# Kernel optimization log

Measured on AMD Instinct MI355X. Metric: run time of the kernel, lower is better.

Reference implementation:

```python
import jax, jax.numpy as jnp
import numpy as np

DIM = 256
NUM_HEADS = 8
KERNEL_SIZES = [7, 7]
DILATIONS = [1, 2]
NUM_SPLITS = 2
HEAD_DIM = DIM // NUM_HEADS
SCALE = HEAD_DIM ** -0.5


def _window_start(L, K, D):
    """NATTEN get_window_start, vectorized over indices 0..L-1 (static numpy)."""
    idx = np.arange(L)
    NH = K // 2
    if D <= 1:
        return np.maximum(idx - NH, 0) + (idx + NH >= L) * (L - idx - NH - 1)
    ni = idx - NH * D
    imodd = idx % D
    a = (L // D) * D
    b = L - a
    edge = np.where(imodd < b, L - b + imodd - 2 * NH * D, a + imodd - K * D)
    return np.where(ni < 0, imodd, np.where(idx + NH * D >= L, edge, ni))


def _pb_start(L, K, D):
    """NATTEN get_pb_start (relative position bias offset), static numpy."""
    idx = np.arange(L)
    NH = K // 2
    if D <= 1:
        return NH + (idx < NH) * (NH - idx) + (idx + NH >= L) * (L - idx - 1 - NH)
    return np.where(idx - NH * D < 0, K - 1 - idx // D,
                    np.where(idx + NH * D >= L, (L - idx - 1) // D, NH))


def _natten2d(q, k, v, rpb, K, D):
    # q,k,v: [B,h,H,W,d]; rpb: [h, 2K-1, 2K-1]
    B, h, H, W, d = q.shape
    ki = _window_start(H, K, D)[:, None] + D * np.arange(K)   # [H,K]
    kj = _window_start(W, K, D)[:, None] + D * np.arange(K)   # [W,K]
    bi = _pb_start(H, K, D)[:, None] + np.arange(K)           # [H,K]
    bj = _pb_start(W, K, D)[:, None] + np.arange(K)           # [W,K]
    kg = jnp.take(jnp.take(k, ki, axis=2), kj, axis=4)        # [B,h,H,K,W,K,d]
    vg = jnp.take(jnp.take(v, ki, axis=2), kj, axis=4)        # [B,h,H,K,W,K,d]
    attn = jnp.einsum('bhijd,bhiujvd->bhijuv', q, kg)         # [B,h,H,W,K,K]
    bias = jnp.take(jnp.take(rpb, bi, axis=1), bj, axis=3)    # [h,H,K,W,K]
    attn = attn + bias.transpose(0, 1, 3, 2, 4)[None]
    attn = jax.nn.softmax(attn.reshape(B, h, H, W, K * K), axis=-1)
    attn = attn.reshape(B, h, H, W, K, K)
    return jnp.einsum('bhijuv,bhiujvd->bhijd', attn, vg)      # [B,h,H,W,d]


def setup_inputs() -> dict:
    key = jax.random.key(0)
    ks = jax.random.split(key, 6)
    B, C, H, W = 2, DIM, 56, 56
    x = jax.random.normal(ks[0], (B, C, H, W), dtype=jnp.float32)
    w_qkv1 = jax.random.normal(ks[1], (3 * C, C), dtype=jnp.float32) * (C ** -0.5)
    w_qkv2 = jax.random.normal(ks[2], (3 * C, 1, 3, 3), dtype=jnp.float32) * (1.0 / 3.0)
    rpb0 = jax.random.truncated_normal(ks[3], -2.0, 2.0,
                                       (NUM_HEADS // NUM_SPLITS, 13, 13), dtype=jnp.float32) * 0.02
    rpb1 = jax.random.truncated_normal(ks[4], -2.0, 2.0,
                                       (NUM_HEADS // NUM_SPLITS, 13, 13), dtype=jnp.float32) * 0.02
    w_proj = jax.random.normal(ks[5], (C, C), dtype=jnp.float32) * (C ** -0.5)
    return {"x": x, "w_qkv1": w_qkv1, "w_qkv2": w_qkv2,
            "rpb0": rpb0, "rpb1": rpb1, "w_proj": w_proj}


def reference(x, w_qkv1, w_qkv2, rpb0, rpb1, w_proj):
    B, C, H, W = x.shape
    # qkv: 1x1 conv (no bias) then depthwise 3x3 conv (no bias)
    y = jnp.einsum('oc,bchw->bohw', w_qkv1, x)
    y = jax.lax.conv_general_dilated(
        y, w_qkv2, window_strides=(1, 1), padding='SAME',
        dimension_numbers=('NCHW', 'OIHW', 'NCHW'), feature_group_count=3 * C)
    # Faithful to torch: raw reshape of [B,3C,H,W] -> [B,H,W,3,nh,hd]
    qkv = y.reshape(B, H, W, 3, NUM_HEADS, HEAD_DIM).transpose(3, 0, 4, 1, 2, 5)
    q, k, v = qkv[0] * SCALE, qkv[1], qkv[2]   # [B,nh,H,W,hd]
    hs = NUM_HEADS // NUM_SPLITS
    rpbs = [rpb0, rpb1]
    outs = []
    for s in range(NUM_SPLITS):
        sl = slice(s * hs, (s + 1) * hs)
        outs.append(_natten2d(q[:, sl], k[:, sl], v[:, sl],
                              rpbs[s], KERNEL_SIZES[s], DILATIONS[s]))
    o = jnp.concatenate(outs, axis=1)                 # [B,nh,H,W,hd]
    o = o.transpose(0, 1, 4, 2, 3).reshape(B, C, H, W)
    return jnp.einsum('oc,bchw->bohw', w_proj, o)
```

## Files before the change

kernel.cpp:

```cpp
#include <hip/hip_runtime.h>
#include <hip/hip_bf16.h>

#define HGT 56
#define WID 56
#define SPA 3136
#define CCH 256
#define C3  768
#define NH  8
#define HD  32
#define YB  2408448
#define ISTR 43008
#define JSTR 768
#define SCALE_Q 0.17677669529663687f

typedef __attribute__((ext_vector_type(8))) short short8;
typedef __attribute__((ext_vector_type(4))) float f32x4;

static __device__ __forceinline__ unsigned short f2bf_bits(float f) {
    __hip_bfloat16 h = __float2bfloat16(f);
    union { __hip_bfloat16 h; unsigned short u; } cv; cv.h = h; return cv.u;
}
static __device__ __forceinline__ float bf_lo(unsigned u) {
    union { unsigned x; float f; } c; c.x = u << 16; return c.f;
}
static __device__ __forceinline__ float bf_hi(unsigned u) {
    union { unsigned x; float f; } c; c.x = u & 0xffff0000u; return c.f;
}
static __device__ __forceinline__ float bfu(unsigned short u) {
    union { unsigned x; float f; } c; c.x = (unsigned)u << 16; return c.f;
}
static __device__ __forceinline__ unsigned pk2bf(float a, float b) {
    return ((unsigned)f2bf_bits(b) << 16) | (unsigned)f2bf_bits(a);
}

__global__ __launch_bounds__(256) void k_cvt(const float* __restrict__ x,
                                             const float* __restrict__ w1,
                                             const float* __restrict__ wp,
                                             __hip_bfloat16* __restrict__ xT,
                                             __hip_bfloat16* __restrict__ w1b,
                                             __hip_bfloat16* __restrict__ wpb) {
    __shared__ __align__(16) __hip_bfloat16 Sl[64][80];
    const int t = threadIdx.x;
    const int z = blockIdx.z;
    if (z == 2) {
        const int gid = (blockIdx.y * 49 + blockIdx.x) * 256 + t;
        for (int i = gid * 4; i < 262144; i += 200704) {
            const float* src;
            __hip_bfloat16* dst;
            if (i < 196608) { src = w1 + i; dst = w1b + i; }
            else            { src = wp + (i - 196608); dst = wpb + (i - 196608); }
            float4 v = *(const float4*)src;
            ushort4 u;
            u.x = f2bf_bits(v.x); u.y = f2bf_bits(v.y);
            u.z = f2bf_bits(v.z); u.w = f2bf_bits(v.w);
            *(ushort4*)dst = u;
        }
        return;
    }
    const int b = z, c0 = blockIdx.y * 64, s0 = blockIdx.x * 64;
    const float* xb = x + (size_t)b * (CCH * SPA);
    const int sq = (t & 15) * 4, cq = (t >> 4) * 4;
    float4 r[4];
#pragma unroll
    for (int rr = 0; rr < 4; ++rr)
        r[rr] = *(const float4*)&xb[(size_t)(c0 + cq + rr) * SPA + s0 + sq];
#pragma unroll
    for (int j = 0; j < 4; ++j) {
        ushort4 u;
        u.x = f2bf_bits(((const float*)&r[0])[j]);
        u.y = f2bf_bits(((const float*)&r[1])[j]);
        u.z = f2bf_bits(((const float*)&r[2])[j]);
        u.w = f2bf_bits(((const float*)&r[3])[j]);
        *(ushort4*)&Sl[sq + j][cq] = u;
    }
    __syncthreads();
    const int srow = t >> 2, cslot = t & 3;
    __hip_bfloat16* dst = &xT[(size_t)b * SPA * CCH + (size_t)(s0 + srow) * CCH + c0];
    short8 v0 = *(const short8*)&Sl[srow][cslot * 8];
    short8 v1 = *(const short8*)&Sl[srow][(cslot + 4) * 8];
    *(short8*)&dst[cslot * 8] = v0;
    *(short8*)&dst[(cslot + 4) * 8] = v1;
}

template<bool OBF>
__global__ __launch_bounds__(256) void k_gemm(const __hip_bfloat16* __restrict__ A,
                                              const __hip_bfloat16* __restrict__ B,
                                              void* __restrict__ Cv, int M) {
    __shared__ __align__(16) short sA[4096];
    __shared__ __align__(16) short sB[4096];
    const int t = threadIdx.x;
    const int lane = t & 63, w = t >> 6;
    const int s0 = blockIdx.x * 64, o0 = blockIdx.y * 64, b = blockIdx.z;
    const __hip_bfloat16* Bb = B + (size_t)b * SPA * CCH;

    const int srow = t >> 3;
    const int scol = (t & 7) ^ (srow & 7);
    const char* gA = (const char*)(A  + (size_t)(o0 + srow) * CCH) + scol * 16;
    const char* gB = (const char*)(Bb + (size_t)(s0 + srow) * CCH) + scol * 16;
    char* lA = (char*)sA + w * 1024;
    char* lB = (char*)sB + w * 1024;

    const int wm = w >> 1, wn = w & 1;
    const int lr = lane & 15, kh = lane >> 4;
    const int ar0 = wm * 32 + lr, ar1 = ar0 + 16;
    const int br0 = wn * 32 + lr, br1 = br0 + 16;

    f32x4 acc[2][2] = {};
    for (int kt = 0; kt < 4; ++kt) {
        __builtin_amdgcn_global_load_lds(
            (const __attribute__((address_space(1))) void*)(gA + kt * 128),
            (__attribute__((address_space(3))) void*)lA, 16, 0, 0);
        __builtin_amdgcn_global_load_lds(
            (const __attribute__((address_space(1))) void*)(gA + 16384 + kt * 128),
            (__attribute__((address_space(3))) void*)(lA + 4096), 16, 0, 0);
        __builtin_amdgcn_global_load_lds(
            (const __attribute__((address_space(1))) void*)(gB + kt * 128),
            (__attribute__((address_space(3))) void*)lB, 16, 0, 0);
        __builtin_amdgcn_global_load_lds(
            (const __attribute__((address_space(1))) void*)(gB + 16384 + kt * 128),
            (__attribute__((address_space(3))) void*)(lB + 4096), 16, 0, 0);
        __syncthreads();
#pragma unroll
        for (int kk = 0; kk < 2; ++kk) {
            const int kg = (kk << 2) | kh;
            short8 a0 = *(const short8*)&sA[(ar0 * 128 + ((kg ^ (ar0 & 7)) << 4)) >> 1];
            short8 a1 = *(const short8*)&sA[(ar1 * 128 + ((kg ^ (ar1 & 7)) << 4)) >> 1];
            short8 b0 = *(const short8*)&sB[(br0 * 128 + ((kg ^ (br0 & 7)) << 4)) >> 1];
            short8 b1 = *(const short8*)&sB[(br1 * 128 + ((kg ^ (br1 & 7)) << 4)) >> 1];
            acc[0][0] = __builtin_amdgcn_mfma_f32_16x16x32_bf16(a0, b0, acc[0][0], 0, 0, 0);
            acc[0][1] = __builtin_amdgcn_mfma_f32_16x16x32_bf16(a0, b1, acc[0][1], 0, 0, 0);
            acc[1][0] = __builtin_amdgcn_mfma_f32_16x16x32_bf16(a1, b0, acc[1][0], 0, 0, 0);
            acc[1][1] = __builtin_amdgcn_mfma_f32_16x16x32_bf16(a1, b1, acc[1][1], 0, 0, 0);
        }
        __syncthreads();
    }
#pragma unroll
    for (int mi = 0; mi < 2; ++mi)
#pragma unroll
        for (int ni = 0; ni < 2; ++ni) {
            const int r0 = o0 + wm * 32 + mi * 16 + kh * 4;
            const int cc = s0 + wn * 32 + ni * 16 + lr;
            if constexpr (OBF) {
                __hip_bfloat16* Cb = (__hip_bfloat16*)Cv + (size_t)b * M * SPA;
#pragma unroll
                for (int q = 0; q < 4; ++q)
                    Cb[(size_t)(r0 + q) * SPA + cc] = __float2bfloat16(acc[mi][ni][q]);
            } else {
                float* Cb = (float*)Cv + (size_t)b * M * SPA;
#pragma unroll
                for (int q = 0; q < 4; ++q)
                    Cb[(size_t)(r0 + q) * SPA + cc] = acc[mi][ni][q];
            }
        }
}

__global__ __launch_bounds__(256) void k_dw(const __hip_bfloat16* __restrict__ y1,
                                            const float* __restrict__ w2,
                                            __hip_bfloat16* __restrict__ y2) {
    int idx = blockIdx.x * 256 + threadIdx.x;
    int tw = idx % 14;
    int rest = idx / 14;
    int h = rest % HGT;
    int bc = rest / HGT;
    int w0 = tw * 4;
    const __hip_bfloat16* in = y1 + (size_t)bc * SPA;
    const float* wt = w2 + (bc % C3) * 9;
    float a0 = 0.f, a1 = 0.f, a2 = 0.f, a3 = 0.f;
#pragma unroll
    for (int dh = -1; dh <= 1; ++dh) {
        int hh = h + dh;
        if (hh < 0 || hh >= HGT) continue;
        const __hip_bfloat16* rp = in + hh * WID + w0;
        ushort4 c4 = *(const ushort4*)rp;
        float c0 = bfu(c4.x), c1 = bfu(c4.y), c2 = bfu(c4.z), c3 = bfu(c4.w);
        float l = (w0 > 0)  ? bfu(*(const unsigned short*)(rp - 1)) : 0.f;
        float r = (w0 < 52) ? bfu(*(const unsigned short*)(rp + 4)) : 0.f;
        float wl = wt[(dh + 1) * 3 + 0];
        float wc = wt[(dh + 1) * 3 + 1];
        float wr = wt[(dh + 1) * 3 + 2];
        a0 += wl * l  + wc * c0 + wr * c1;
        a1 += wl * c0 + wc * c1 + wr * c2;
        a2 += wl * c1 + wc * c2 + wr * c3;
        a3 += wl * c2 + wc * c3 + wr * r;
    }
    ushort4 o;
    o.x = f2bf_bits(a0); o.y = f2bf_bits(a1);
    o.z = f2bf_bits(a2); o.w = f2bf_bits(a3);
    *(ushort4*)(y2 + (size_t)bc * SPA + h * WID + w0) = o;
}

template<int D>
__device__ __forceinline__ void attn7_body(short* __restrict__ sK,
                                           short* __restrict__ sVT,
                                           short* __restrict__ sQ,
                                           short* __restrict__ sP,
                                           float* __restrict__ sEB,
                                           const __hip_bfloat16* __restrict__ y2,
                                           const float* __restrict__ rpb,
                                           __hip_bfloat16* __restrict__ opre,
                                           int b, int head, int i, int hsub) {
    const int tid = threadIdx.x;
    const int lane = tid & 63, w = tid >> 6;
    const int lr = lane & 15, kh = lane >> 4;

    int wsi, pbi;
    if (D == 1) {
        wsi = (i < 3) ? 0 : ((i > 52) ? 49 : i - 3);
        pbi = (i < 3) ? 6 - i : ((i > 52) ? 55 - i : 3);
    } else {
        wsi = (i < 6) ? (i & 1) : ((i >= 50) ? 42 + (i & 1) : i - 6);
        pbi = (i < 6) ? 6 - (i >> 1) : ((i >= 50) ? (55 - i) >> 1 : 3);
    }

    const __hip_bfloat16* base  = y2 + (size_t)b * YB + head * HD;
    const __hip_bfloat16* kbase = base + CCH     + wsi * ISTR;
    const __hip_bfloat16* vbase = base + 2 * CCH + wsi * ISTR;
    const __hip_bfloat16* qbase = base + i * ISTR;

    for (int f = tid; f < 1792; f += 256) {
        int u = f >> 8, rem = f & 255, kj = rem >> 2, slot = rem & 3;
        int kjc = (kj > 55) ? 55 : kj;
        const __hip_bfloat16* src = kbase + u * (D * ISTR) + kjc * JSTR + ((slot ^ (kj & 3)) << 3);
        char* dst = (char*)sK + (size_t)(f - lane) * 16;
        __builtin_amdgcn_global_load_lds(
            (const __attribute__((address_space(1))) void*)src,
            (__attribute__((address_space(3))) void*)dst, 16, 0, 0);
    }
    {
        int jq = tid >> 2, slot = tid & 3;
        int jqc = (jq > 55) ? 55 : jq;
        const __hip_bfloat16* src = qbase + jqc * JSTR + ((slot ^ (jq & 3)) << 3);
        char* dst = (char*)sQ + (size_t)(tid - lane) * 16;
        __builtin_amdgcn_global_load_lds(
            (const __attribute__((address_space(1))) void*)src,
            (__attribute__((address_space(3))) void*)dst, 16, 0, 0);
    }
    for (int f = tid; f < 1568; f += 256) {
        int u = f / 224, rem = f - u * 224;
        int dq = rem / 28, kjp = rem - dq * 28;
        const __hip_bfloat16* g0 = vbase + u * (D * ISTR) + (2 * kjp) * JSTR + dq * 4;
        ushort4 va = *(const ushort4*)g0;
        ushort4 vb = *(const ushort4*)(g0 + JSTR);
#pragma unroll
        for (int e = 0; e < 4; ++e) {
            int d = dq * 4 + e;
            unsigned pk = ((unsigned)((&vb.x)[e]) << 16) | (unsigned)((&va.x)[e]);
            int row = u * 32 + d;
            int byt = row * 128 + ((((kjp >> 2) ^ (d & 7)) << 4)) + (kjp & 3) * 4;
            *(unsigned*)((char*)sVT + byt) = pk;
        }
    }
    if (tid < 224) {
        int u = tid >> 5, d = tid & 31;
        int row = u * 32 + d;
        int byt = row * 128 + ((7 ^ (d & 7)) << 4);
        *(short8*)((char*)sVT + byt) = (short8){0, 0, 0, 0, 0, 0, 0, 0};
    }
    if (tid < 91) {
        int u = tid / 13, r = tid - u * 13;
        sEB[tid] = __expf(rpb[hsub * 169 + (pbi + u) * 13 + r]);
    }
    __syncthreads();

    const int j = w * 16 + lr;
    int wsj;
    if (D == 1) wsj = (j < 3) ? 0 : ((j > 52) ? 49 : j - 3);
    else        wsj = (j < 6) ? (j & 1) : ((j >= 50) ? 42 + (j & 1) : j - 6);

    short8 qf = *(const short8*)((char*)sQ + j * 64 + ((kh ^ (j & 3)) << 4));

    float ssum = 0.f;
    f32x4 oacc0 = {0.f, 0.f, 0.f, 0.f};
    f32x4 oacc1 = {0.f, 0.f, 0.f, 0.f};
    short* sPw = sP + w * 2048;

#pragma unroll
    for (int u = 0; u < 7; ++u) {
        char* sPb = (char*)(sPw + (u & 1) * 1024);
        f32x4 s[4];
#pragma unroll
        for (int Mt = 0; Mt < 4; ++Mt) {
            int kjrow = u * 64 + Mt * 16 + lr;
            short8 kf = *(const short8*)((char*)sK + kjrow * 64 + ((kh ^ (lr & 3)) << 4));
            s[Mt] = __builtin_amdgcn_mfma_f32_16x16x32_bf16(kf, qf,
                        (f32x4){0.f, 0.f, 0.f, 0.f}, 0, 0, 0);
        }
#pragma unroll
        for (int Mt = 0; Mt < 4; ++Mt) {
            const int kjb = Mt * 16 + (kh << 2);
            float ev[4];
#pragma unroll
            for (int q = 0; q < 4; ++q) {
                int kj = kjb + q;
                int rel = kj - j;
                int din = kj - wsj;
                bool valid = (din >= 0) && (din <= 6 * D);
                if (D == 2) valid = valid && ((rel & 1) == 0);
                int r = (D == 1) ? (rel + 6) : ((rel >> 1) + 6);
                r = r < 0 ? 0 : (r > 12 ? 12 : r);
                float ex = __expf(s[Mt][q] * SCALE_Q) * sEB[u * 13 + r];
                ev[q] = valid ? ex : 0.f;
                ssum += ev[q];
            }
            uint2 pk2;
            pk2.x = pk2bf(ev[0], ev[1]);
            pk2.y = pk2bf(ev[2], ev[3]);
            int g = Mt * 2 + (kh >> 1);
            int byt = lr * 128 + (((g ^ (lr & 7)) << 4)) + (kh & 1) * 8;
            *(uint2*)(sPb + byt) = pk2;
        }
        __syncthreads();
#pragma unroll
        for (int Kt = 0; Kt < 2; ++Kt) {
            short8 pf = *(const short8*)(sPb + lr * 128 + ((((Kt * 4 + kh) ^ (lr & 7)) << 4)));
            {
                int row = u * 32 + lr;
                short8 vf = *(const short8*)((char*)sVT + row * 128 +
                              ((((Kt * 4 + kh) ^ (lr & 7)) << 4)));
                oacc0 = __builtin_amdgcn_mfma_f32_16x16x32_bf16(vf, pf, oacc0, 0, 0, 0);
            }
            {
                int row = u * 32 + 16 + lr;
                short8 vf = *(const short8*)((char*)sVT + row * 128 +
                              ((((Kt * 4 + kh) ^ (lr & 7)) << 4)));
                oacc1 = __builtin_amdgcn_mfma_f32_16x16x32_bf16(vf, pf, oacc1, 0, 0, 0);
            }
        }
    }

    ssum += __shfl_xor(ssum, 16);
    ssum += __shfl_xor(ssum, 32);

    if (j < 56) {
        const float rinv = __frcp_rn(ssum);
        const size_t ob = (size_t)b * (SPA * CCH) + (size_t)(i * WID + j) * CCH
                          + head * HD + (kh << 2);
        uint2 p0, p1;
        p0.x = pk2bf(oacc0[0] * rinv, oacc0[1] * rinv);
        p0.y = pk2bf(oacc0[2] * rinv, oacc0[3] * rinv);
        p1.x = pk2bf(oacc1[0] * rinv, oacc1[1] * rinv);
        p1.y = pk2bf(oacc1[2] * rinv, oacc1[3] * rinv);
        *(uint2*)&opre[ob]      = p0;
        *(uint2*)&opre[ob + 16] = p1;
    }
}

__global__ __launch_bounds__(256) void k_attn7(const __hip_bfloat16* __restrict__ y2,
                                               const float* __restrict__ rpb0,
                                               const float* __restrict__ rpb1,
                                               __hip_bfloat16* __restrict__ opre) {
    __shared__ __align__(16) short sK[14336];
    __shared__ __align__(16) short sVT[14336];
    __shared__ __align__(16) short sQ[2048];
    __shared__ __align__(16) short sP[8192];
    __shared__ float sEB[91];
    const int i = blockIdx.x;
    const int bh = blockIdx.y;
    const int b = bh >> 3, head = bh & 7;
    if (head < 4)
        attn7_body<1>(sK, sVT, sQ, sP, sEB, y2, rpb0, opre, b, head, i, head);
    else
        attn7_body<2>(sK, sVT, sQ, sP, sEB, y2, rpb1, opre, b, head, i, head - 4);
}

extern "C" void kernel_launch(void* const* d_in, const int* in_sizes, int n_in,
                              void* d_out, int out_size, void* d_ws, size_t ws_size,
                              hipStream_t stream) {
    const float* x    = (const float*)d_in[0];
    const float* w1   = (const float*)d_in[1];
    const float* w2   = (const float*)d_in[2];
    const float* rpb0 = (const float*)d_in[3];
    const float* rpb1 = (const float*)d_in[4];
    const float* wp   = (const float*)d_in[5];
    float* out = (float*)d_out;

    float* p = (float*)d_ws;
    __hip_bfloat16* y1b  = (__hip_bfloat16*)p;
    __hip_bfloat16* y2b  = (__hip_bfloat16*)(p + YB);
    __hip_bfloat16* xT   = (__hip_bfloat16*)(p + 2 * YB);
    __hip_bfloat16* opre = xT;
    __hip_bfloat16* w1b  = (__hip_bfloat16*)(p + 2 * YB + 802816);
    __hip_bfloat16* wpb  = (__hip_bfloat16*)(p + 2 * YB + 802816 + 98304);

    k_cvt<<<dim3(49, 4, 3), 256, 0, stream>>>(x, w1, wp, xT, w1b, wpb);
    k_gemm<true><<<dim3(49, 12, 2), 256, 0, stream>>>(w1b, xT, (void*)y1b, C3);
    k_dw<<<dim3(4704), 256, 0, stream>>>(y1b, w2, y2b);
    k_attn7<<<dim3(HGT, 2 * NH), 256, 0, stream>>>(y2b, rpb0, rpb1, opre);
    k_gemm<false><<<dim3(49, 4, 2), 256, 0, stream>>>(wpb, opre, (void*)out, CCH);
}
```

Measured before the change: 58.53 us.

## Fuse fp32-to-bf16 conversion into GEMM tile loads and drop the conversion kernel

New measurement: 61.39 us. 4.9% more time.

```diff
diff --git a/kernel.cpp b/kernel.cpp
--- a/kernel.cpp
+++ b/kernel.cpp
@@ -20,85 +20,28 @@
     __hip_bfloat16 h = __float2bfloat16(f);
     union { __hip_bfloat16 h; unsigned short u; } cv; cv.h = h; return cv.u;
 }
-static __device__ __forceinline__ float bf_lo(unsigned u) {
-    union { unsigned x; float f; } c; c.x = u << 16; return c.f;
-}
-static __device__ __forceinline__ float bf_hi(unsigned u) {
-    union { unsigned x; float f; } c; c.x = u & 0xffff0000u; return c.f;
-}
 static __device__ __forceinline__ float bfu(unsigned short u) {
     union { unsigned x; float f; } c; c.x = (unsigned)u << 16; return c.f;
 }
 static __device__ __forceinline__ unsigned pk2bf(float a, float b) {
     return ((unsigned)f2bf_bits(b) << 16) | (unsigned)f2bf_bits(a);
 }
-
-__global__ __launch_bounds__(256) void k_cvt(const float* __restrict__ x,
-                                             const float* __restrict__ w1,
-                                             const float* __restrict__ wp,
-                                             __hip_bfloat16* __restrict__ xT,
-                                             __hip_bfloat16* __restrict__ w1b,
-                                             __hip_bfloat16* __restrict__ wpb) {
-    __shared__ __align__(16) __hip_bfloat16 Sl[64][80];
-    const int t = threadIdx.x;
-    const int z = blockIdx.z;
-    if (z == 2) {
-        const int gid = (blockIdx.y * 49 + blockIdx.x) * 256 + t;
-        for (int i = gid * 4; i < 262144; i += 200704) {
-            const float* src;
-            __hip_bfloat16* dst;
-            if (i < 196608) { src = w1 + i; dst = w1b + i; }
-            else            { src = wp + (i - 196608); dst = wpb + (i - 196608); }
-            float4 v = *(const float4*)src;
-            ushort4 u;
-            u.x = f2bf_bits(v.x); u.y = f2bf_bits(v.y);
-            u.z = f2bf_bits(v.z); u.w = f2bf_bits(v.w);
-            *(ushort4*)dst = u;
-        }
-        return;
-    }
-    const int b = z, c0 = blockIdx.y * 64, s0 = blockIdx.x * 64;
-    const float* xb = x + (size_t)b * (CCH * SPA);
-    const int sq = (t & 15) * 4, cq = (t >> 4) * 4;
-    float4 r[4];
-#pragma unroll
-    for (int rr = 0; rr < 4; ++rr)
-        r[rr] = *(const float4*)&xb[(size_t)(c0 + cq + rr) * SPA + s0 + sq];
-#pragma unroll
-    for (int j = 0; j < 4; ++j) {
-        ushort4 u;
-        u.x = f2bf_bits(((const float*)&r[0])[j]);
-        u.y = f2bf_bits(((const float*)&r[1])[j]);
-        u.z = f2bf_bits(((const float*)&r[2])[j]);
-        u.w = f2bf_bits(((const float*)&r[3])[j]);
-        *(ushort4*)&Sl[sq + j][cq] = u;
-    }
-    __syncthreads();
-    const int srow = t >> 2, cslot = t & 3;
-    __hip_bfloat16* dst = &xT[(size_t)b * SPA * CCH + (size_t)(s0 + srow) * CCH + c0];
-    short8 v0 = *(const short8*)&Sl[srow][cslot * 8];
-    short8 v1 = *(const short8*)&Sl[srow][(cslot + 4) * 8];
-    *(short8*)&dst[cslot * 8] = v0;
-    *(short8*)&dst[(cslot + 4) * 8] = v1;
-}
-
-template<bool OBF>
-__global__ __launch_bounds__(256) void k_gemm(const __hip_bfloat16* __restrict__ A,
-                                              const __hip_bfloat16* __restrict__ B,
-                                              void* __restrict__ Cv, int M) {
+static __device__ __forceinline__ unsigned long long pk4bf(float a, float b, float c, float d) {
+    return ((unsigned long long)pk2bf(c, d) << 32) | (unsigned long long)pk2bf(a, b);
+}
+
+__global__ __launch_bounds__(256) void k_gemm_qkv(const float* __restrict__ w1,
+                                                  const float* __restrict__ x,
+                                                  __hip_bfloat16* __restrict__ y1) {
     __shared__ __align__(16) short sA[4096];
     __shared__ __align__(16) short sB[4096];
     const int t = threadIdx.x;
     const int lane = t & 63, w = t >> 6;
     const int s0 = blockIdx.x * 64, o0 = blockIdx.y * 64, b = blockIdx.z;
-    const __hip_bfloat16* Bb = B + (size_t)b * SPA * CCH;
-
-    const int srow = t >> 3;
-    const int scol = (t & 7) ^ (srow & 7);
-    const char* gA = (const char*)(A  + (size_t)(o0 + srow) * CCH) + scol * 16;
-    const char* gB = (const char*)(Bb + (size_t)(s0 + srow) * CCH) + scol * 16;
-    char* lA = (char*)sA + w * 1024;
-    char* lB = (char*)sB + w * 1024;
+    const float* xb = x + (size_t)b * (CCH * SPA);
+
+    const int orow = t >> 2, ac = (t & 3) * 16;
+    const int cq = (t >> 4) * 4, sq = (t & 15) * 4;
 
     const int wm = w >> 1, wn = w & 1;
     const int lr = lane & 15, kh = lane >> 4;
@@ -107,18 +50,33 @@
 
     f32x4 acc[2][2] = {};
     for (int kt = 0; kt < 4; ++kt) {
-        __builtin_amdgcn_global_load_lds(
-            (const __attribute__((address_space(1))) void*)(gA + kt * 128),
-            (__attribute__((address_space(3))) void*)lA, 16, 0, 0);
-        __builtin_amdgcn_global_load_lds(
-            (const __attribute__((address_space(1))) void*)(gA + 16384 + kt * 128),
-            (__attribute__((address_space(3))) void*)(lA + 4096), 16, 0, 0);
-        __builtin_amdgcn_global_load_lds(
-            (const __attribute__((address_space(1))) void*)(gB + kt * 128),
-            (__attribute__((address_space(3))) void*)lB, 16, 0, 0);
-        __builtin_amdgcn_global_load_lds(
-            (const __attribute__((address_space(1))) void*)(gB + 16384 + kt * 128),
-            (__attribute__((address_space(3))) void*)(lB + 4096), 16, 0, 0);
+        const int c0 = kt * 64;
+        float4 a4[4], b4[4];
+#pragma unroll
+        for (int r = 0; r < 4; ++r)
+            a4[r] = *(const float4*)&w1[(size_t)(o0 + orow) * CCH + c0 + ac + r * 4];
+#pragma unroll
+        for (int r = 0; r < 4; ++r)
+            b4[r] = *(const float4*)&xb[(size_t)(c0 + cq + r) * SPA + s0 + sq];
+        __syncthreads();
+#pragma unroll
+        for (int r = 0; r < 4; ++r) {
+            const int byt = ac * 2 + r * 8;
+            const int slot = byt >> 4, half = (byt >> 3) & 1;
+            *(unsigned long long*)((char*)sA + orow * 128 +
+                (((slot ^ (orow & 7)) << 4) | (half << 3))) =
+                pk4bf(a4[r].x, a4[r].y, a4[r].z, a4[r].w);
+        }
+#pragma unroll
+        for (int e = 0; e < 4; ++e) {
+            const int srow = sq + e;
+            const int byt = cq * 2;
+            const int slot = byt >> 4, half = (byt >> 3) & 1;
+            *(unsigned long long*)((char*)sB + srow * 128 +
+                (((slot ^ (srow & 7)) << 4) | (half << 3))) =
+                pk4bf(((const float*)&b4[0])[e], ((const float*)&b4[1])[e],
+                      ((const float*)&b4[2])[e], ((const float*)&b4[3])[e]);
+        }
         __syncthreads();
 #pragma unroll
         for (int kk = 0; kk < 2; ++kk) {
@@ -132,25 +90,87 @@
             acc[1][0] = __builtin_amdgcn_mfma_f32_16x16x32_bf16(a1, b0, acc[1][0], 0, 0, 0);
             acc[1][1] = __builtin_amdgcn_mfma_f32_16x16x32_bf16(a1, b1, acc[1][1], 0, 0, 0);
         }
-        __syncthreads();
-    }
+    }
+    __hip_bfloat16* Cb = y1 + (size_t)b * C3 * SPA;
 #pragma unroll
     for (int mi = 0; mi < 2; ++mi)
 #pragma unroll
         for (int ni = 0; ni < 2; ++ni) {
             const int r0 = o0 + wm * 32 + mi * 16 + kh * 4;
             const int cc = s0 + wn * 32 + ni * 16 + lr;
-            if constexpr (OBF) {
-                __hip_bfloat16* Cb = (__hip_bfloat16*)Cv + (size_t)b * M * SPA;
-#pragma unroll
-                for (int q = 0; q < 4; ++q)
-                    Cb[(size_t)(r0 + q) * SPA + cc] = __float2bfloat16(acc[mi][ni][q]);
-            } else {
-                float* Cb = (float*)Cv + (size_t)b * M * SPA;
-#pragma unroll
-                for (int q = 0; q < 4; ++q)
-                    Cb[(size_t)(r0 + q) * SPA + cc] = acc[mi][ni][q];
-            }
+#pragma unroll
+            for (int q = 0; q < 4; ++q)
+                Cb[(size_t)(r0 + q) * SPA + cc] = __float2bfloat16(acc[mi][ni][q]);
+        }
+}
+
+__global__ __launch_bounds__(256) void k_gemm_proj(const float* __restrict__ wp,
+                                                   const __hip_bfloat16* __restrict__ B,
+                                                   float* __restrict__ out) {
+    __shared__ __align__(16) short sA[4096];
+    __shared__ __align__(16) short sB[4096];
+    const int t = threadIdx.x;
+    const int lane = t & 63, w = t >> 6;
+    const int s0 = blockIdx.x * 64, o0 = blockIdx.y * 64, b = blockIdx.z;
+    const __hip_bfloat16* Bb = B + (size_t)b * SPA * CCH;
+
+    const int orow = t >> 2, ac = (t & 3) * 16;
+    const int srow = t >> 3;
+    const int scol = (t & 7) ^ (srow & 7);
+    const char* gB = (const char*)(Bb + (size_t)(s0 + srow) * CCH) + scol * 16;
+    char* lB = (char*)sB + w * 1024;
+
+    const int wm = w >> 1, wn = w & 1;
+    const int lr = lane & 15, kh = lane >> 4;
+    const int ar0 = wm * 32 + lr, ar1 = ar0 + 16;
+    const int br0 = wn * 32 + lr, br1 = br0 + 16;
+
+    f32x4 acc[2][2] = {};
+    for (int kt = 0; kt < 4; ++kt) {
+        const int c0 = kt * 64;
+        float4 a4[4];
+#pragma unroll
+        for (int r = 0; r < 4; ++r)
+            a4[r] = *(const float4*)&wp[(size_t)(o0 + orow) * CCH + c0 + ac + r * 4];
+        __syncthreads();
+        __builtin_amdgcn_global_load_lds(
+            (const __attribute__((address_space(1))) void*)(gB + kt * 128),
+            (__attribute__((address_space(3))) void*)lB, 16, 0, 0);
+        __builtin_amdgcn_global_load_lds(
+            (const __attribute__((address_space(1))) void*)(gB + 16384 + kt * 128),
+            (__attribute__((address_space(3))) void*)(lB + 4096), 16, 0, 0);
+#pragma unroll
+        for (int r = 0; r < 4; ++r) {
+            const int byt = ac * 2 + r * 8;
+            const int slot = byt >> 4, half = (byt >> 3) & 1;
+            *(unsigned long long*)((char*)sA + orow * 128 +
+                (((slot ^ (orow & 7)) << 4) | (half << 3))) =
+                pk4bf(a4[r].x, a4[r].y, a4[r].z, a4[r].w);
+        }
+        __syncthreads();
+#pragma unroll
+        for (int kk = 0; kk < 2; ++kk) {
+            const int kg = (kk << 2) | kh;
+            short8 a0 = *(const short8*)&sA[(ar0 * 128 + ((kg ^ (ar0 & 7)) << 4)) >> 1];
+            short8 a1 = *(const short8*)&sA[(ar1 * 128 + ((kg ^ (ar1 & 7)) << 4)) >> 1];
+            short8 b0 = *(const short8*)&sB[(br0 * 128 + ((kg ^ (br0 & 7)) << 4)) >> 1];
+            short8 b1 = *(const short8*)&sB[(br1 * 128 + ((kg ^ (br1 & 7)) << 4)) >> 1];
+            acc[0][0] = __builtin_amdgcn_mfma_f32_16x16x32_bf16(a0, b0, acc[0][0], 0, 0, 0);
+            acc[0][1] = __builtin_amdgcn_mfma_f32_16x16x32_bf16(a0, b1, acc[0][1], 0, 0, 0);
+            acc[1][0] = __builtin_amdgcn_mfma_f32_16x16x32_bf16(a1, b0, acc[1][0], 0, 0, 0);
+            acc[1][1] = __builtin_amdgcn_mfma_f32_16x16x32_bf16(a1, b1, acc[1][1], 0, 0, 0);
+        }
+    }
+    float* Cb = out + (size_t)b * CCH * SPA;
+#pragma unroll
+    for (int mi = 0; mi < 2; ++mi)
+#pragma unroll
+        for (int ni = 0; ni < 2; ++ni) {
+            const int r0 = o0 + wm * 32 + mi * 16 + kh * 4;
+            const int cc = s0 + wn * 32 + ni * 16 + lr;
+#pragma unroll
+            for (int q = 0; q < 4; ++q)
+                Cb[(size_t)(r0 + q) * SPA + cc] = acc[mi][ni][q];
         }
 }
 
@@ -309,7 +329,8 @@
             int byt = lr * 128 + (((g ^ (lr & 7)) << 4)) + (kh & 1) * 8;
             *(uint2*)(sPb + byt) = pk2;
         }
-        __syncthreads();
+        asm volatile("s_waitcnt lgkmcnt(0)" ::: "memory");
+        __builtin_amdgcn_sched_barrier(0);
 #pragma unroll
         for (int Kt = 0; Kt < 2; ++Kt) {
             short8 pf = *(const short8*)(sPb + lr * 128 + ((((Kt * 4 + kh) ^ (lr & 7)) << 4)));
@@ -377,14 +398,10 @@
     float* p = (float*)d_ws;
     __hip_bfloat16* y1b  = (__hip_bfloat16*)p;
     __hip_bfloat16* y2b  = (__hip_bfloat16*)(p + YB);
-    __hip_bfloat16* xT   = (__hip_bfloat16*)(p + 2 * YB);
-    __hip_bfloat16* opre = xT;
-    __hip_bfloat16* w1b  = (__hip_bfloat16*)(p + 2 * YB + 802816);
-    __hip_bfloat16* wpb  = (__hip_bfloat16*)(p + 2 * YB + 802816 + 98304);
-
-    k_cvt<<<dim3(49, 4, 3), 256, 0, stream>>>(x, w1, wp, xT, w1b, wpb);
-    k_gemm<true><<<dim3(49, 12, 2), 256, 0, stream>>>(w1b, xT, (void*)y1b, C3);
+    __hip_bfloat16* opre = (__hip_bfloat16*)(p + 2 * YB);
+
+    k_gemm_qkv<<<dim3(49, 12, 2), 256, 0, stream>>>(w1, x, y1b);
     k_dw<<<dim3(4704), 256, 0, stream>>>(y1b, w2, y2b);
     k_attn7<<<dim3(HGT, 2 * NH), 256, 0, stream>>>(y2b, rpb0, rpb1, opre);
-    k_gemm<false><<<dim3(49, 4, 2), 256, 0, stream>>>(wpb, opre, (void*)out, CCH);
-}
+    k_gemm_proj<<<dim3(49, 4, 2), 256, 0, stream>>>(wp, opre, out);
+}
```

## Fuse x transpose/convert into QKV GEMM and drop syncthreads in attention P stage

Applied to the files above, without the earlier changes.

Result: slower. 61.78 us (+5.6%).

```diff
diff --git a/kernel.cpp b/kernel.cpp
--- a/kernel.cpp
+++ b/kernel.cpp
@@ -20,76 +20,118 @@
     __hip_bfloat16 h = __float2bfloat16(f);
     union { __hip_bfloat16 h; unsigned short u; } cv; cv.h = h; return cv.u;
 }
-static __device__ __forceinline__ float bf_lo(unsigned u) {
-    union { unsigned x; float f; } c; c.x = u << 16; return c.f;
-}
-static __device__ __forceinline__ float bf_hi(unsigned u) {
-    union { unsigned x; float f; } c; c.x = u & 0xffff0000u; return c.f;
-}
 static __device__ __forceinline__ float bfu(unsigned short u) {
     union { unsigned x; float f; } c; c.x = (unsigned)u << 16; return c.f;
 }
 static __device__ __forceinline__ unsigned pk2bf(float a, float b) {
     return ((unsigned)f2bf_bits(b) << 16) | (unsigned)f2bf_bits(a);
 }
-
-__global__ __launch_bounds__(256) void k_cvt(const float* __restrict__ x,
-                                             const float* __restrict__ w1,
-                                             const float* __restrict__ wp,
-                                             __hip_bfloat16* __restrict__ xT,
-                                             __hip_bfloat16* __restrict__ w1b,
-                                             __hip_bfloat16* __restrict__ wpb) {
-    __shared__ __align__(16) __hip_bfloat16 Sl[64][80];
+static __device__ __forceinline__ unsigned long long pk4bf(float a, float b, float c, float d) {
+    return ((unsigned long long)pk2bf(c, d) << 32) | (unsigned long long)pk2bf(a, b);
+}
+
+__global__ __launch_bounds__(256) void k_cvtw(const float* __restrict__ w1,
+                                              const float* __restrict__ wp,
+                                              __hip_bfloat16* __restrict__ w1b,
+                                              __hip_bfloat16* __restrict__ wpb) {
+    int i = (blockIdx.x * 256 + threadIdx.x) * 4;
+    const float* src;
+    __hip_bfloat16* dst;
+    if (i < 196608) { src = w1 + i; dst = w1b + i; }
+    else            { src = wp + (i - 196608); dst = wpb + (i - 196608); }
+    float4 v = *(const float4*)src;
+    ushort4 u;
+    u.x = f2bf_bits(v.x); u.y = f2bf_bits(v.y);
+    u.z = f2bf_bits(v.z); u.w = f2bf_bits(v.w);
+    *(ushort4*)dst = u;
+}
+
+__global__ __launch_bounds__(256, 2) void k_qkv(const __hip_bfloat16* __restrict__ w1b,
+                                                const float* __restrict__ x,
+                                                __hip_bfloat16* __restrict__ y1) {
+    __shared__ __align__(16) short sB[16384];
+    __shared__ __align__(16) short sA[16384];
     const int t = threadIdx.x;
-    const int z = blockIdx.z;
-    if (z == 2) {
-        const int gid = (blockIdx.y * 49 + blockIdx.x) * 256 + t;
-        for (int i = gid * 4; i < 262144; i += 200704) {
-            const float* src;
-            __hip_bfloat16* dst;
-            if (i < 196608) { src = w1 + i; dst = w1b + i; }
-            else            { src = wp + (i - 196608); dst = wpb + (i - 196608); }
-            float4 v = *(const float4*)src;
-            ushort4 u;
-            u.x = f2bf_bits(v.x); u.y = f2bf_bits(v.y);
-            u.z = f2bf_bits(v.z); u.w = f2bf_bits(v.w);
-            *(ushort4*)dst = u;
-        }
-        return;
-    }
-    const int b = z, c0 = blockIdx.y * 64, s0 = blockIdx.x * 64;
+    const int lane = t & 63, wv = t >> 6;
+    const int s0 = blockIdx.x * 64, oh = blockIdx.y, b = blockIdx.z;
     const float* xb = x + (size_t)b * (CCH * SPA);
+
     const int sq = (t & 15) * 4, cq = (t >> 4) * 4;
-    float4 r[4];
-#pragma unroll
-    for (int rr = 0; rr < 4; ++rr)
-        r[rr] = *(const float4*)&xb[(size_t)(c0 + cq + rr) * SPA + s0 + sq];
-#pragma unroll
-    for (int j = 0; j < 4; ++j) {
-        ushort4 u;
-        u.x = f2bf_bits(((const float*)&r[0])[j]);
-        u.y = f2bf_bits(((const float*)&r[1])[j]);
-        u.z = f2bf_bits(((const float*)&r[2])[j]);
-        u.w = f2bf_bits(((const float*)&r[3])[j]);
-        *(ushort4*)&Sl[sq + j][cq] = u;
-    }
-    __syncthreads();
-    const int srow = t >> 2, cslot = t & 3;
-    __hip_bfloat16* dst = &xT[(size_t)b * SPA * CCH + (size_t)(s0 + srow) * CCH + c0];
-    short8 v0 = *(const short8*)&Sl[srow][cslot * 8];
-    short8 v1 = *(const short8*)&Sl[srow][(cslot + 4) * 8];
-    *(short8*)&dst[cslot * 8] = v0;
-    *(short8*)&dst[(cslot + 4) * 8] = v1;
-}
-
-template<bool OBF>
-__global__ __launch_bounds__(256) void k_gemm(const __hip_bfloat16* __restrict__ A,
+#pragma unroll
+    for (int cc0 = 0; cc0 < 256; cc0 += 64) {
+        float4 r[4];
+#pragma unroll
+        for (int rr = 0; rr < 4; ++rr)
+            r[rr] = *(const float4*)&xb[(size_t)(cc0 + cq + rr) * SPA + s0 + sq];
+#pragma unroll
+        for (int e = 0; e < 4; ++e) {
+            const int srow = sq + e, cc = cc0 + cq;
+            const int g = cc >> 3, half = (cc >> 2) & 1;
+            *(unsigned long long*)((char*)sB + srow * 512 +
+                (((g ^ (srow & 7)) << 4) | (half << 3))) =
+                pk4bf(((const float*)&r[0])[e], ((const float*)&r[1])[e],
+                      ((const float*)&r[2])[e], ((const float*)&r[3])[e]);
+        }
+    }
+
+    const int wm = wv >> 1, wn = wv & 1;
+    const int lr = lane & 15, kh = lane >> 4;
+    const int ar0 = wm * 32 + lr, ar1 = ar0 + 16;
+    const int br0 = wn * 32 + lr, br1 = br0 + 16;
+    const int arow8 = t >> 5;
+    const int agl = t & 31;
+
+    for (int ot = 0; ot < 6; ++ot) {
+        const int o0 = (oh * 6 + ot) * 64;
+        __syncthreads();
+#pragma unroll
+        for (int r = 0; r < 8; ++r) {
+            const int row = r * 8 + arow8;
+            const int gs = agl ^ (row & 7);
+            const __hip_bfloat16* src = w1b + (size_t)(o0 + row) * CCH + gs * 8;
+            char* dst = (char*)sA + r * 4096 + wv * 1024;
+            __builtin_amdgcn_global_load_lds(
+                (const __attribute__((address_space(1))) void*)src,
+                (__attribute__((address_space(3))) void*)dst, 16, 0, 0);
+        }
+        __syncthreads();
+        f32x4 acc[2][2] = {};
+#pragma unroll
+        for (int kt = 0; kt < 4; ++kt) {
+#pragma unroll
+            for (int kk = 0; kk < 2; ++kk) {
+                const int g = kt * 8 + (kk << 2) + kh;
+                short8 a0 = *(const short8*)((char*)sA + ar0 * 512 + ((g ^ (ar0 & 7)) << 4));
+                short8 a1 = *(const short8*)((char*)sA + ar1 * 512 + ((g ^ (ar1 & 7)) << 4));
+                short8 b0 = *(const short8*)((char*)sB + br0 * 512 + ((g ^ (br0 & 7)) << 4));
+                short8 b1 = *(const short8*)((char*)sB + br1 * 512 + ((g ^ (br1 & 7)) << 4));
+                acc[0][0] = __builtin_amdgcn_mfma_f32_16x16x32_bf16(a0, b0, acc[0][0], 0, 0, 0);
+                acc[0][1] = __builtin_amdgcn_mfma_f32_16x16x32_bf16(a0, b1, acc[0][1], 0, 0, 0);
+                acc[1][0] = __builtin_amdgcn_mfma_f32_16x16x32_bf16(a1, b0, acc[1][0], 0, 0, 0);
+                acc[1][1] = __builtin_amdgcn_mfma_f32_16x16x32_bf16(a1, b1, acc[1][1], 0, 0, 0);
+            }
+        }
+        __hip_bfloat16* Cb = y1 + (size_t)b * C3 * SPA;
+#pragma unroll
+        for (int mi = 0; mi < 2; ++mi)
+#pragma unroll
+            for (int ni = 0; ni < 2; ++ni) {
+                const int r0 = o0 + wm * 32 + mi * 16 + kh * 4;
+                const int cc = s0 + wn * 32 + ni * 16 + lr;
+#pragma unroll
+                for (int q = 0; q < 4; ++q)
+                    Cb[(size_t)(r0 + q) * SPA + cc] = __float2bfloat16(acc[mi][ni][q]);
+            }
+    }
+}
+
+__global__ __launch_bounds__(256) void k_proj(const __hip_bfloat16* __restrict__ A,
                                               const __hip_bfloat16* __restrict__ B,
-                                              void* __restrict__ Cv, int M) {
+                                              float* __restrict__ C) {
     __shared__ __align__(16) short sA[4096];
     __shared__ __align__(16) short sB[4096];
     const int t = threadIdx.x;
-    const int lane = t & 63, w = t >> 6;
+    const int lane = t & 63, wv = t >> 6;
     const int s0 = blockIdx.x * 64, o0 = blockIdx.y * 64, b = blockIdx.z;
     const __hip_bfloat16* Bb = B + (size_t)b * SPA * CCH;
 
@@ -97,10 +139,10 @@
     const int scol = (t & 7) ^ (srow & 7);
     const char* gA = (const char*)(A  + (size_t)(o0 + srow) * CCH) + scol * 16;
     const char* gB = (const char*)(Bb + (size_t)(s0 + srow) * CCH) + scol * 16;
-    char* lA = (char*)sA + w * 1024;
-    char* lB = (char*)sB + w * 1024;
-
-    const int wm = w >> 1, wn = w & 1;
+    char* lA = (char*)sA + wv * 1024;
+    char* lB = (char*)sB + wv * 1024;
+
+    const int wm = wv >> 1, wn = wv & 1;
     const int lr = lane & 15, kh = lane >> 4;
     const int ar0 = wm * 32 + lr, ar1 = ar0 + 16;
     const int br0 = wn * 32 + lr, br1 = br0 + 16;
@@ -134,23 +176,16 @@
         }
         __syncthreads();
     }
+    float* Cb = C + (size_t)b * CCH * SPA;
 #pragma unroll
     for (int mi = 0; mi < 2; ++mi)
 #pragma unroll
         for (int ni = 0; ni < 2; ++ni) {
             const int r0 = o0 + wm * 32 + mi * 16 + kh * 4;
             const int cc = s0 + wn * 32 + ni * 16 + lr;
-            if constexpr (OBF) {
-                __hip_bfloat16* Cb = (__hip_bfloat16*)Cv + (size_t)b * M * SPA;
-#pragma unroll
-                for (int q = 0; q < 4; ++q)
-                    Cb[(size_t)(r0 + q) * SPA + cc] = __float2bfloat16(acc[mi][ni][q]);
-            } else {
-                float* Cb = (float*)Cv + (size_t)b * M * SPA;
-#pragma unroll
-                for (int q = 0; q < 4; ++q)
-                    Cb[(size_t)(r0 + q) * SPA + cc] = acc[mi][ni][q];
-            }
+#pragma unroll
+            for (int q = 0; q < 4; ++q)
+                Cb[(size_t)(r0 + q) * SPA + cc] = acc[mi][ni][q];
         }
 }
 
@@ -200,7 +235,7 @@
                                            __hip_bfloat16* __restrict__ opre,
                                            int b, int head, int i, int hsub) {
     const int tid = threadIdx.x;
-    const int lane = tid & 63, w = tid >> 6;
+    const int lane = tid & 63, wv = tid >> 6;
     const int lr = lane & 15, kh = lane >> 4;
 
     int wsi, pbi;
@@ -262,7 +297,7 @@
     }
     __syncthreads();
 
-    const int j = w * 16 + lr;
+    const int j = wv * 16 + lr;
     int wsj;
     if (D == 1) wsj = (j < 3) ? 0 : ((j > 52) ? 49 : j - 3);
     else        wsj = (j < 6) ? (j & 1) : ((j >= 50) ? 42 + (j & 1) : j - 6);
@@ -272,7 +307,7 @@
     float ssum = 0.f;
     f32x4 oacc0 = {0.f, 0.f, 0.f, 0.f};
     f32x4 oacc1 = {0.f, 0.f, 0.f, 0.f};
-    short* sPw = sP + w * 2048;
+    short* sPw = sP + wv * 2048;
 
 #pragma unroll
     for (int u = 0; u < 7; ++u) {
@@ -309,7 +344,8 @@
             int byt = lr * 128 + (((g ^ (lr & 7)) << 4)) + (kh & 1) * 8;
             *(uint2*)(sPb + byt) = pk2;
         }
-        __syncthreads();
+        asm volatile("s_waitcnt lgkmcnt(0)" ::: "memory");
+        __builtin_amdgcn_sched_barrier(0);
 #pragma unroll
         for (int Kt = 0; Kt < 2; ++Kt) {
             short8 pf = *(const short8*)(sPb + lr * 128 + ((((Kt * 4 + kh) ^ (lr & 7)) << 4)));
@@ -377,14 +413,13 @@
     float* p = (float*)d_ws;
     __hip_bfloat16* y1b  = (__hip_bfloat16*)p;
     __hip_bfloat16* y2b  = (__hip_bfloat16*)(p + YB);
-    __hip_bfloat16* xT   = (__hip_bfloat16*)(p + 2 * YB);
-    __hip_bfloat16* opre = xT;
+    __hip_bfloat16* opre = (__hip_bfloat16*)(p + 2 * YB);
     __hip_bfloat16* w1b  = (__hip_bfloat16*)(p + 2 * YB + 802816);
     __hip_bfloat16* wpb  = (__hip_bfloat16*)(p + 2 * YB + 802816 + 98304);
 
-    k_cvt<<<dim3(49, 4, 3), 256, 0, stream>>>(x, w1, wp, xT, w1b, wpb);
-    k_gemm<true><<<dim3(49, 12, 2), 256, 0, stream>>>(w1b, xT, (void*)y1b, C3);
+    k_cvtw<<<dim3(256), 256, 0, stream>>>(w1, wp, w1b, wpb);
+    k_qkv<<<dim3(49, 2, 2), 256, 0, stream>>>(w1b, x, y1b);
     k_dw<<<dim3(4704), 256, 0, stream>>>(y1b, w2, y2b);
     k_attn7<<<dim3(HGT, 2 * NH), 256, 0, stream>>>(y2b, rpb0, rpb1, opre);
-    k_gemm<false><<<dim3(49, 4, 2), 256, 0, stream>>>(wpb, opre, (void*)out, CCH);
-}
+    k_proj<<<dim3(49, 4, 2), 256, 0, stream>>>(wpb, opre, out);
+}
```
